# Optimization experiments

Hardware: AMD Instinct MI355X
Metric: run time of the kernel (lower is better)

Reference implementation:

```python
import jax, jax.numpy as jnp
import numpy as np

GROUP = 5  # in-group size implied by `expected_in = indices.shape[1] * 5`


def setup_inputs() -> dict:
    key = jax.random.key(0)
    k1, k2, k3, k4 = jax.random.split(key, 4)
    T, IN, OUT, G, C, K = 64, 4100, 12288, 820, 2, 256
    x = jax.random.normal(k1, (T, IN), dtype=jnp.float32)
    indices = jax.random.randint(k2, (OUT, G, C), 0, K, dtype=jnp.int32)
    codebooks = (jax.random.normal(k3, (C, K, GROUP), dtype=jnp.float32) * 0.05).astype(jnp.float16)
    scales = jax.random.uniform(k4, (OUT,), dtype=jnp.float32, minval=0.5, maxval=1.5)
    return {"x": x, "indices": indices, "codebooks": codebooks, "scales": scales}


def reference(x, indices, codebooks, scales):
    orig_shape = x.shape
    x_flat = x.reshape(-1, orig_shape[-1])
    expected_in = indices.shape[1] * GROUP
    pad = expected_in - x_flat.shape[1]
    if pad > 0:
        x_flat = jnp.pad(x_flat, ((0, 0), (0, pad)))
    # safety scaling (fp16 overflow guard), as in the torch module
    x_max = jnp.maximum(jnp.abs(x_flat).max(), 1.0) * 8.0
    cb_max = jnp.maximum(jnp.abs(codebooks).astype(jnp.float32).max(), 1.0)
    x_safe = (x_flat / x_max).astype(jnp.float16)
    cb_safe = (codebooks.astype(jnp.float32) / cb_max).astype(jnp.float16)
    # additive-codebook dequant: W[o, g] = sum_c cb_safe[c, indices[o,g,c], :]
    C = cb_safe.shape[0]
    gathered = cb_safe[jnp.arange(C)[None, None, :], indices]  # (O, G, C, GROUP) fp16
    W = gathered.sum(axis=2).reshape(indices.shape[0], -1)     # (O, expected_in) fp16
    out = jnp.einsum('ti,oi->to', x_safe, W, preferred_element_type=jnp.float32)
    out = out * x_max.astype(jnp.float32) * cb_max
    out = out * scales[None, :]
    out = jnp.nan_to_num(out, nan=0.0, posinf=0.0, neginf=0.0)
    return out.reshape(*orig_shape[:-1], -1).astype(x.dtype)
```

## Files before the change

### kernel.cpp

```cpp
#include <hip/hip_runtime.h>
#include <hip/hip_fp16.h>
#include <cstdint>

#define T_DIM 64
#define IN_DIM 4100
#define OUT_DIM 12288
#define G_DIM 820
#define KCODE 256
#define GRP 5
#define KP 6560
#define KB32 205
#define CHUNKS 41
#define CH_G 20
#define CH_K 160
#define KSPLIT 4
#define NBLK 192
#define LDS_STRIDE 168

typedef _Float16 f16x8 __attribute__((ext_vector_type(8)));
typedef float f32x4 __attribute__((ext_vector_type(4)));

__device__ float g_pmax[256];
__device__ float g_cbmax;
__device__ float g_xmax;
__device__ __align__(16) _Float16 g_cbq[2 * KCODE * 8];
__device__ __align__(16) _Float16 g_xA[4 * KB32 * 64 * 8];
__device__ __align__(16) float g_part[KSPLIT * T_DIM * OUT_DIM];

__device__ __forceinline__ float block_reduce_max(float m, float* sm) {
    for (int off = 32; off > 0; off >>= 1)
        m = fmaxf(m, __shfl_down(m, off));
    int tid = threadIdx.x;
    if ((tid & 63) == 0) sm[tid >> 6] = m;
    __syncthreads();
    float r = fmaxf(fmaxf(sm[0], sm[1]), fmaxf(sm[2], sm[3]));
    __syncthreads();
    return r;
}

__global__ void __launch_bounds__(256) k1_absmax_cb(const float* __restrict__ x,
                                                    const void* __restrict__ cbraw) {
    __shared__ float sm[4];
    int tid = threadIdx.x, bid = blockIdx.x;
    float m = 0.f;
    for (int i = bid * 256 + tid; i < T_DIM * IN_DIM; i += 256 * 256)
        m = fmaxf(m, fabsf(x[i]));
    float r = block_reduce_max(m, sm);
    if (tid == 0) g_pmax[bid] = r;

    if (bid == 0) {
        unsigned u0 = *(const unsigned*)cbraw;
        bool is_f32 = (((u0 >> 23) & 0xFF) >= 100);
        float mm = 0.f;
        for (int i = tid; i < 2 * KCODE * GRP; i += 256) {
            float v = is_f32 ? ((const float*)cbraw)[i]
                             : (float)((const _Float16*)cbraw)[i];
            mm = fmaxf(mm, fabsf(v));
        }
        float cbm = fmaxf(block_reduce_max(mm, sm), 1.0f);
        if (tid == 0) g_cbmax = cbm;
        for (int e = tid; e < 2 * KCODE; e += 256) {
            f16x8 v = {};
            #pragma unroll
            for (int j = 0; j < GRP; ++j) {
                float w = is_f32 ? ((const float*)cbraw)[e * GRP + j]
                                 : (float)((const _Float16*)cbraw)[e * GRP + j];
                v[j] = (_Float16)(w / cbm);
            }
            *(f16x8*)&g_cbq[e * 8] = v;
        }
    }
}

__global__ void __launch_bounds__(256) k2_quant(const float* __restrict__ x) {
    __shared__ float sm[4];
    int tid = threadIdx.x;
    float xm = fmaxf(block_reduce_max(g_pmax[tid], sm), 1.0f) * 8.0f;
    if (blockIdx.x == 0 && tid == 0) g_xmax = xm;

    int gt = blockIdx.x * 256 + tid;
    int lane = gt & 63;
    int rest = gt >> 6;
    int kb32 = rest % KB32;
    int t16 = rest / KB32;
    int r16 = lane & 15, q = lane >> 4;
    int t = t16 * 16 + r16;
    int g = kb32 * 4 + q;
    const float* xp = x + (size_t)t * IN_DIM + g * GRP;
    f16x8 v = {};
    #pragma unroll
    for (int j = 0; j < GRP; ++j) v[j] = (_Float16)(xp[j] / xm);
    *(f16x8*)&g_xA[(size_t)gt * 8] = v;
}

__global__ void __launch_bounds__(256) k3_gemm(const int* __restrict__ indices) {
    __shared__ alignas(16) _Float16 w_lds[64 * LDS_STRIDE];
    __shared__ f16x8 cb_sh[2 * KCODE];

    int tid = threadIdx.x;
    int nb = blockIdx.x % NBLK;
    int ksp = blockIdx.x / NBLK;
    int n_base = nb * 64;

    for (int e = tid; e < 2 * KCODE; e += 256)
        cb_sh[e] = *(const f16x8*)&g_cbq[e * 8];

    int sro[5], sgl[5];
    #pragma unroll
    for (int j = 0; j < 5; ++j) {
        int s = tid + j * 256;
        sro[j] = s / 20; sgl[j] = s - sro[j] * 20;
    }

    const int c0 = (CHUNKS * ksp) / KSPLIT;
    const int c1 = (CHUNKS * (ksp + 1)) / KSPLIT;
    const int wid = tid >> 6, lane = tid & 63;
    const int q = lane >> 4, r16 = lane & 15;

    f32x4 acc[4] = {};
    int2 idxr[5];
    uint4 ar[5];
    auto prefetch = [&](int c) {
        int g0 = c * CH_G, kb = c * 5;
        #pragma unroll
        for (int j = 0; j < 5; ++j) {
            ar[j] = *(const uint4*)&g_xA[(size_t)((wid * KB32 + kb + j) * 64 + lane) * 8];
            idxr[j] = *(const int2*)&indices[(size_t)(n_base + sro[j]) * (G_DIM * 2)
                                             + (size_t)(g0 + sgl[j]) * 2];
        }
    };

    prefetch(c0);
    __syncthreads();

    for (int c = c0; c < c1; ++c) {
        #pragma unroll
        for (int j = 0; j < 5; ++j) {
            f16x8 w = cb_sh[idxr[j].x] + cb_sh[KCODE + idxr[j].y];
            *(f16x8*)&w_lds[sro[j] * LDS_STRIDE + sgl[j] * 8] = w;
        }
        uint4 acur[5];
        #pragma unroll
        for (int j = 0; j < 5; ++j) acur[j] = ar[j];
        __syncthreads();
        if (c + 1 < c1) prefetch(c + 1);
        #pragma unroll
        for (int kk = 0; kk < 5; ++kk) {
            f16x8 a = *(f16x8*)&acur[kk];
            #pragma unroll
            for (int nt = 0; nt < 4; ++nt) {
                f16x8 b = *(const f16x8*)&w_lds[(nt * 16 + r16) * LDS_STRIDE + kk * 32 + q * 8];
                acc[nt] = __builtin_amdgcn_mfma_f32_16x16x32_f16(a, b, acc[nt], 0, 0, 0);
            }
        }
        __syncthreads();
    }

    float* outp = g_part + (size_t)ksp * (T_DIM * OUT_DIM);
    #pragma unroll
    for (int nt = 0; nt < 4; ++nt) {
        #pragma unroll
        for (int rr = 0; rr < 4; ++rr) {
            int t = wid * 16 + q * 4 + rr;
            int o = n_base + nt * 16 + r16;
            outp[t * OUT_DIM + o] = acc[nt][rr];
        }
    }
}

__global__ void __launch_bounds__(256) k4_final(const float* __restrict__ scales,
                                                float* __restrict__ out) {
    int i4 = blockIdx.x * 256 + threadIdx.x;
    if (i4 >= T_DIM * OUT_DIM / 4) return;
    float s = g_xmax * g_cbmax;
    const f32x4* p = (const f32x4*)g_part;
    const int Q = T_DIM * OUT_DIM / 4;
    f32x4 v0 = p[i4], v1 = p[Q + i4], v2 = p[2 * Q + i4], v3 = p[3 * Q + i4];
    int o4 = i4 % (OUT_DIM / 4);
    f32x4 sc = *(const f32x4*)&scales[o4 * 4];
    f32x4 r;
    #pragma unroll
    for (int j = 0; j < 4; ++j) {
        float v = (v0[j] + v1[j] + v2[j] + v3[j]) * s * sc[j];
        if (!isfinite(v)) v = 0.f;
        r[j] = v;
    }
    ((f32x4*)out)[i4] = r;
}

extern "C" void kernel_launch(void* const* d_in, const int* in_sizes, int n_in,
                              void* d_out, int out_size, void* d_ws, size_t ws_size,
                              hipStream_t stream) {
    const float* x = (const float*)d_in[0];
    const int* indices = (const int*)d_in[1];
    const void* cbraw = (const void*)d_in[2];
    const float* scales = (const float*)d_in[3];
    float* out = (float*)d_out;
    (void)d_ws; (void)ws_size; (void)n_in; (void)in_sizes; (void)out_size;

    k1_absmax_cb<<<256, 256, 0, stream>>>(x, cbraw);
    k2_quant<<<205, 256, 0, stream>>>(x);
    k3_gemm<<<NBLK * KSPLIT, 256, 0, stream>>>(indices);
    k4_final<<<T_DIM * OUT_DIM / 4 / 256, 256, 0, stream>>>(scales, out);
}
```

Before: 147.8 us.

## Switch GEMM to 32x32x16 MFMA with double-buffered LDS weight tiles

Replaces the 16x16x32 MFMA tiling with 32x32x16 MFMA, where each wave computes one 32x32 output tile (2 waves over tokens, 2 over outputs). The quantized x layout is reorganized into 16-wide k-slices to match the new operand layout. The LDS weight tile becomes double-buffered so the trailing barrier per chunk can be dropped. Activation loads are now issued inside the loop rather than prefetched a chunk ahead. This could expose global load latency, and it raises register pressure from holding 10 uint4 values.

```diff
diff --git a/kernel.cpp b/kernel.cpp
--- a/kernel.cpp
+++ b/kernel.cpp
@@ -9,22 +9,24 @@
 #define KCODE 256
 #define GRP 5
 #define KP 6560
-#define KB32 205
+#define KB16 410
 #define CHUNKS 41
 #define CH_G 20
 #define CH_K 160
+#define KS_PER_CH 10
 #define KSPLIT 4
 #define NBLK 192
 #define LDS_STRIDE 168
 
 typedef _Float16 f16x8 __attribute__((ext_vector_type(8)));
 typedef float f32x4 __attribute__((ext_vector_type(4)));
+typedef float f32x16 __attribute__((ext_vector_type(16)));
 
 __device__ float g_pmax[256];
 __device__ float g_cbmax;
 __device__ float g_xmax;
 __device__ __align__(16) _Float16 g_cbq[2 * KCODE * 8];
-__device__ __align__(16) _Float16 g_xA[4 * KB32 * 64 * 8];
+__device__ __align__(16) _Float16 g_xA[2 * KB16 * 64 * 8];
 __device__ __align__(16) float g_part[KSPLIT * T_DIM * OUT_DIM];
 
 __device__ __forceinline__ float block_reduce_max(float m, float* sm) {
@@ -81,11 +83,11 @@
     int gt = blockIdx.x * 256 + tid;
     int lane = gt & 63;
     int rest = gt >> 6;
-    int kb32 = rest % KB32;
-    int t16 = rest / KB32;
-    int r16 = lane & 15, q = lane >> 4;
-    int t = t16 * 16 + r16;
-    int g = kb32 * 4 + q;
+    int kb16 = rest % KB16;
+    int t2 = rest / KB16;
+    int r32 = lane & 31, h = lane >> 5;
+    int t = t2 * 32 + r32;
+    int g = kb16 * 2 + h;
     const float* xp = x + (size_t)t * IN_DIM + g * GRP;
     f16x8 v = {};
     #pragma unroll
@@ -94,7 +96,7 @@
 }
 
 __global__ void __launch_bounds__(256) k3_gemm(const int* __restrict__ indices) {
-    __shared__ alignas(16) _Float16 w_lds[64 * LDS_STRIDE];
+    __shared__ alignas(16) _Float16 w_lds[2][64 * LDS_STRIDE];
     __shared__ f16x8 cb_sh[2 * KCODE];
 
     int tid = threadIdx.x;
@@ -115,56 +117,53 @@
     const int c0 = (CHUNKS * ksp) / KSPLIT;
     const int c1 = (CHUNKS * (ksp + 1)) / KSPLIT;
     const int wid = tid >> 6, lane = tid & 63;
-    const int q = lane >> 4, r16 = lane & 15;
-
-    f32x4 acc[4] = {};
+    const int wo = wid & 1, wt = wid >> 1;
+    const int r32 = lane & 31, h = lane >> 5;
+
+    f32x16 acc = {};
     int2 idxr[5];
-    uint4 ar[5];
-    auto prefetch = [&](int c) {
-        int g0 = c * CH_G, kb = c * 5;
-        #pragma unroll
-        for (int j = 0; j < 5; ++j) {
-            ar[j] = *(const uint4*)&g_xA[(size_t)((wid * KB32 + kb + j) * 64 + lane) * 8];
+    auto prefetch_idx = [&](int c) {
+        int g0 = c * CH_G;
+        #pragma unroll
+        for (int j = 0; j < 5; ++j)
             idxr[j] = *(const int2*)&indices[(size_t)(n_base + sro[j]) * (G_DIM * 2)
                                              + (size_t)(g0 + sgl[j]) * 2];
-        }
     };
 
-    prefetch(c0);
+    prefetch_idx(c0);
     __syncthreads();
 
     for (int c = c0; c < c1; ++c) {
+        const int buf = c & 1;
+        uint4 ar[KS_PER_CH];
+        #pragma unroll
+        for (int ks = 0; ks < KS_PER_CH; ++ks)
+            ar[ks] = *(const uint4*)
+                &g_xA[(size_t)((wt * KB16 + c * KS_PER_CH + ks) * 64 + lane) * 8];
+
         #pragma unroll
         for (int j = 0; j < 5; ++j) {
             f16x8 w = cb_sh[idxr[j].x] + cb_sh[KCODE + idxr[j].y];
-            *(f16x8*)&w_lds[sro[j] * LDS_STRIDE + sgl[j] * 8] = w;
-        }
-        uint4 acur[5];
-        #pragma unroll
-        for (int j = 0; j < 5; ++j) acur[j] = ar[j];
+            *(f16x8*)&w_lds[buf][sro[j] * LDS_STRIDE + sgl[j] * 8] = w;
+        }
         __syncthreads();
-        if (c + 1 < c1) prefetch(c + 1);
-        #pragma unroll
-        for (int kk = 0; kk < 5; ++kk) {
-            f16x8 a = *(f16x8*)&acur[kk];
-            #pragma unroll
-            for (int nt = 0; nt < 4; ++nt) {
-                f16x8 b = *(const f16x8*)&w_lds[(nt * 16 + r16) * LDS_STRIDE + kk * 32 + q * 8];
-                acc[nt] = __builtin_amdgcn_mfma_f32_16x16x32_f16(a, b, acc[nt], 0, 0, 0);
-            }
-        }
-        __syncthreads();
+        if (c + 1 < c1) prefetch_idx(c + 1);
+
+        #pragma unroll
+        for (int ks = 0; ks < KS_PER_CH; ++ks) {
+            f16x8 b = *(const f16x8*)
+                &w_lds[buf][(wo * 32 + r32) * LDS_STRIDE + ks * 16 + h * 8];
+            acc = __builtin_amdgcn_mfma_f32_32x32x16_f16(*(f16x8*)&ar[ks], b, acc, 0, 0, 0);
+        }
     }
 
     float* outp = g_part + (size_t)ksp * (T_DIM * OUT_DIM);
-    #pragma unroll
-    for (int nt = 0; nt < 4; ++nt) {
-        #pragma unroll
-        for (int rr = 0; rr < 4; ++rr) {
-            int t = wid * 16 + q * 4 + rr;
-            int o = n_base + nt * 16 + r16;
-            outp[t * OUT_DIM + o] = acc[nt][rr];
-        }
+    int o = n_base + wo * 32 + r32;
+    #pragma unroll
+    for (int reg = 0; reg < 16; ++reg) {
+        int row = (reg & 3) + 8 * (reg >> 2) + 4 * h;
+        int t = wt * 32 + row;
+        outp[(size_t)t * OUT_DIM + o] = acc[reg];
     }
 }
 
```

New measurement: 149.6 us. Within noise of the previous version (+1.2%).
